# Kernel optimization log

Hardware: AMD Instinct MI355X
Metric: run time of the kernel (lower is better)

The kernel has to match this reference:

```python
import jax, jax.numpy as jnp
import numpy as np

NEMBED, EMBED_DIM, HID_DIM, OUT_DIM, NUM_CLASSES = 128, 64, 128, 128, 2
BATCH, TEAM = 2048, 5
N_OPS = 8


def setup_inputs() -> dict:
    key = jax.random.key(0)
    ks = jax.random.split(key, 8)
    w_eq = np.sqrt(2.0 / (EMBED_DIM + HID_DIM + N_OPS))
    return {
        "x": jax.random.randint(ks[0], (BATCH, 2, TEAM), 0, NEMBED, dtype=jnp.int32),
        "embed": jax.random.normal(ks[1], (NEMBED, EMBED_DIM), jnp.float32) * 0.1,
        "coefs1": jax.random.normal(ks[2], (EMBED_DIM, HID_DIM, N_OPS), jnp.float32) * w_eq,
        "bias1": jnp.zeros((HID_DIM,), jnp.float32),
        "wout1": jax.random.normal(ks[3], (HID_DIM, OUT_DIM), jnp.float32) * np.sqrt(1.0 / HID_DIM),
        "bout1": jnp.zeros((OUT_DIM,), jnp.float32),
        "coefs2": jax.random.normal(ks[4], (EMBED_DIM, HID_DIM, N_OPS), jnp.float32) * w_eq,
        "bias2": jnp.zeros((HID_DIM,), jnp.float32),
        "wout2": jax.random.normal(ks[5], (HID_DIM, OUT_DIM), jnp.float32) * np.sqrt(1.0 / HID_DIM),
        "bout2": jnp.zeros((OUT_DIM,), jnp.float32),
        "fcw": jax.random.normal(ks[6], (2 * OUT_DIM, NCLS := NUM_CLASSES and 2 * OUT_DIM and NUM_CLASSES), jnp.float32) * np.sqrt(1.0 / (2 * OUT_DIM)),
        "fcb": jnp.zeros((NUM_CLASSES,), jnp.float32),
    }


def eset_ops_3_to_3(t):
    # t: (N, D, m, m, m). 8 equivariant basis ops: keep-or-(sum&broadcast) each axis.
    # Pooled ops are kept with singleton dims; broadcasting happens after the
    # channel contraction (cheaper, same math as expand-then-contract).
    s1 = t.sum(-3, keepdims=True)
    s2 = t.sum(-2, keepdims=True)
    s3 = t.sum(-1, keepdims=True)
    s12 = t.sum((-3, -2), keepdims=True)
    s13 = t.sum((-3, -1), keepdims=True)
    s23 = t.sum((-2, -1), keepdims=True)
    sall = t.sum((-3, -2, -1), keepdims=True)
    return [t, s1, s2, s3, s12, s13, s23, sall]


def eq3_layer(t, coefs, bias):
    # coefs: (D_in, D_out, 8); output (N, D_out, m, m, m)
    ops = eset_ops_3_to_3(t)
    out = 0.0
    for b, op in enumerate(ops):
        out = out + jnp.einsum('ndijk,ds->nsijk', op, coefs[:, :, b])
    return out + bias[None, :, None, None, None]


def setnet3to3(t, coefs, bias, wout, bout):
    h = jax.nn.relu(eq3_layer(t, coefs, bias))          # (N, H, m, m, m)
    return jnp.einsum('nsijk,so->nijko', h, wout) + bout  # (N, m, m, m, out_dim)


def reference(x, embed, coefs1, bias1, wout1, bout1, coefs2, bias2, wout2, bout2, fcw, fcb):
    e1 = jax.nn.relu(embed[x[:, 0]])  # (N, 5, D)
    e2 = jax.nn.relu(embed[x[:, 1]])
    t1 = jnp.einsum('bid,bjd,bkd->bdijk', e1, e1, e1)  # (N, D, 5, 5, 5)
    t2 = jnp.einsum('bid,bjd,bkd->bdijk', e2, e2, e2)
    o1 = setnet3to3(t1, coefs1, bias1, wout1, bout1)
    o2 = setnet3to3(t2, coefs2, bias2, wout2, bout2)
    t1e = jax.nn.relu(o1.mean(axis=(1, 2, 3)))  # (N, out_dim)
    t2e = jax.nn.relu(o2.mean(axis=(1, 2, 3)))
    z = jnp.concatenate([t1e, t2e], axis=-1)    # dropout_prob=0 / eval mode: no-op
    return z @ fcw + fcb
```

## Files before the change

### kernel.cpp

```cpp
#include <hip/hip_runtime.h>


typedef __attribute__((ext_vector_type(8))) short bf16x8;
typedef __attribute__((ext_vector_type(4))) float f32x4;

#define DEV __device__ __forceinline__

DEV constexpr int pid2(int a, int b) {
  int x = a < b ? a : b;
  int y = a < b ? b : a;
  return x * (9 - x) / 2 + y;
}
DEV constexpr int tid3(int i, int j, int k) {
  int a = i, b = j, c = k, t;
  if (a > b) { t = a; a = b; b = t; }
  if (b > c) { t = b; b = c; c = t; }
  if (a > b) { t = a; a = b; b = t; }
  return a * (a * a - 18 * a + 107) / 6 + (b - a) * (11 - a - b) / 2 + (c - b);
}

DEV ushort f2bf(float f) {
  unsigned u = __builtin_bit_cast(unsigned, f);
  return (ushort)((u + 0x7FFFu + ((u >> 16) & 1u)) >> 16);
}

__global__ __launch_bounds__(256)
void cvt_coefs_kernel(const float* __restrict__ c1, const float* __restrict__ c2,
                      ushort* __restrict__ ct) {
  const int idx = blockIdx.x * 256 + threadIdx.x;
  const int d    = idx & 63;
  const int s    = (idx >> 6) & 127;
  const int b    = (idx >> 13) & 7;
  const int side = idx >> 16;
  const float* src = side ? c2 : c1;
  ct[idx] = f2bf(src[(d * 128 + s) * 8 + b]);
}


__global__ __launch_bounds__(256, 2)
void dota2_eq3_mfma(const int* __restrict__ x, const float* __restrict__ embed,
                    const float* __restrict__ bias1, const float* __restrict__ wout1,
                    const float* __restrict__ bout1,
                    const float* __restrict__ bias2, const float* __restrict__ wout2,
                    const float* __restrict__ bout2,
                    const float* __restrict__ fcw, const float* __restrict__ fcb,
                    const ushort* __restrict__ ct, float* __restrict__ out)
{
  __shared__ __align__(16) ushort FT[2][80][72];
  __shared__ __align__(16) float  OUT[128][100];
  __shared__ float hbarL[2][128];
  __shared__ float zL[256];

  const int n   = blockIdx.x;
  const int tid = threadIdx.x;
  const int w   = tid >> 6;
  const int l   = tid & 63;
  const int grp = l >> 4;
  const int lc  = l & 15;

  {
    unsigned long long* f8 = (unsigned long long*)&FT[0][0][0];
    #pragma unroll 4
    for (int i = tid; i < 2880; i += 256) f8[i] = 0ULL;
  }
  __syncthreads();

  if ((tid & 127) < 64) {
    const int side = tid >> 7;
    const int d = tid & 63;
    const int* xn = x + n * 10 + side * 5;
    float v[5];
    #pragma unroll
    for (int i = 0; i < 5; ++i) v[i] = fmaxf(embed[xn[i] * 64 + d], 0.f);
    const float S  = v[0] + v[1] + v[2] + v[3] + v[4];
    const float S2 = S * S;
    const float S3 = S2 * S;
    float p2[15];
    {
      int c2 = 0;
      #pragma unroll
      for (int a = 0; a < 5; ++a)
        #pragma unroll
        for (int b = a; b < 5; ++b) { p2[c2] = v[a] * v[b]; ++c2; }
    }
    ushort* colp = &FT[side][0][d];
    {
      int c3 = 0;
      #pragma unroll
      for (int a = 0; a < 5; ++a)
        #pragma unroll
        for (int b = a; b < 5; ++b)
          #pragma unroll
          for (int c = b; c < 5; ++c) { colp[c3 * 72] = f2bf(p2[pid2(a, b)] * v[c]); ++c3; }
    }
    #pragma unroll
    for (int t = 0; t < 15; ++t) colp[(48 + t) * 72] = f2bf(S * p2[t]);
    #pragma unroll
    for (int i = 0; i < 5; ++i)  colp[(64 + i) * 72] = f2bf(S2 * v[i]);
    colp[69 * 72] = f2bf(S3);
  }
  __syncthreads();

  #pragma unroll 1
  for (int side = 0; side < 2; ++side) {
    const ushort* CTs = ct + side * (8 * 128 * 64);

    auto afrag = [&](int b, int s0, int h) -> bf16x8 {
      const ushort* rp = CTs + (b * 128 + s0 + lc) * 64;
      return *(const bf16x8*)(rp + 32 * h + 8 * grp);
    };
    auto bfrag = [&](int t0, int h) -> bf16x8 {
      return *(const bf16x8*)(&FT[side][t0 + lc][32 * h + 8 * grp]);
    };
    auto dwrite = [&](const f32x4& acc, int s0, int colbase, int nvalid) {
      if (lc < nvalid) {
        float* p = &OUT[s0 + 4 * grp][colbase + lc];
        p[0] = acc[0]; p[100] = acc[1]; p[200] = acc[2]; p[300] = acc[3];
      }
    };

    {
      const bf16x8 A00 = afrag(0, 32 * w,      0), A01 = afrag(0, 32 * w,      1);
      const bf16x8 A10 = afrag(0, 32 * w + 16, 0), A11 = afrag(0, 32 * w + 16, 1);
      #pragma unroll
      for (int nt = 0; nt < 3; ++nt) {
        const bf16x8 B0 = bfrag(nt * 16, 0), B1 = bfrag(nt * 16, 1);
        const int nvalid = (nt == 2) ? 3 : 16;
        f32x4 acc0 = {0.f, 0.f, 0.f, 0.f};
        acc0 = __builtin_amdgcn_mfma_f32_16x16x32_bf16(A00, B0, acc0, 0, 0, 0);
        acc0 = __builtin_amdgcn_mfma_f32_16x16x32_bf16(A01, B1, acc0, 0, 0, 0);
        dwrite(acc0, 32 * w, nt * 16, nvalid);
        f32x4 acc1 = {0.f, 0.f, 0.f, 0.f};
        acc1 = __builtin_amdgcn_mfma_f32_16x16x32_bf16(A10, B0, acc1, 0, 0, 0);
        acc1 = __builtin_amdgcn_mfma_f32_16x16x32_bf16(A11, B1, acc1, 0, 0, 0);
        dwrite(acc1, 32 * w + 16, nt * 16, nvalid);
      }
    }
    {
      const bf16x8 B0 = bfrag(48, 0), B1 = bfrag(48, 1);
      #pragma unroll
      for (int b = 1; b <= 3; ++b)
        #pragma unroll
        for (int u = 0; u < 2; ++u) {
          const int s0 = 32 * w + 16 * u;
          const bf16x8 A0 = afrag(b, s0, 0), A1 = afrag(b, s0, 1);
          f32x4 acc = {0.f, 0.f, 0.f, 0.f};
          acc = __builtin_amdgcn_mfma_f32_16x16x32_bf16(A0, B0, acc, 0, 0, 0);
          acc = __builtin_amdgcn_mfma_f32_16x16x32_bf16(A1, B1, acc, 0, 0, 0);
          dwrite(acc, s0, 35 + (b - 1) * 15, 15);
        }
    }
    {
      const bf16x8 B0 = bfrag(64, 0), B1 = bfrag(64, 1);
      #pragma unroll
      for (int b = 4; b <= 6; ++b)
        #pragma unroll
        for (int u = 0; u < 2; ++u) {
          const int s0 = 32 * w + 16 * u;
          const bf16x8 A0 = afrag(b, s0, 0), A1 = afrag(b, s0, 1);
          f32x4 acc = {0.f, 0.f, 0.f, 0.f};
          acc = __builtin_amdgcn_mfma_f32_16x16x32_bf16(A0, B0, acc, 0, 0, 0);
          acc = __builtin_amdgcn_mfma_f32_16x16x32_bf16(A1, B1, acc, 0, 0, 0);
          dwrite(acc, s0, 80 + (b - 4) * 5, 5);
        }
      #pragma unroll
      for (int u = 0; u < 2; ++u) {
        const int s0 = 32 * w + 16 * u;
        const bf16x8 A0 = afrag(7, s0, 0), A1 = afrag(7, s0, 1);
        f32x4 acc = {0.f, 0.f, 0.f, 0.f};
        acc = __builtin_amdgcn_mfma_f32_16x16x32_bf16(A0, B0, acc, 0, 0, 0);
        acc = __builtin_amdgcn_mfma_f32_16x16x32_bf16(A1, B1, acc, 0, 0, 0);
        if (lc == 5) {
          float* p = &OUT[s0 + 4 * grp][95];
          p[0] = acc[0]; p[100] = acc[1]; p[200] = acc[2]; p[300] = acc[3];
        }
      }
    }
    __syncthreads();

    if (tid < 128) {
      const int s = tid;
      float T[96];
      const f32x4* rp = (const f32x4*)(&OUT[s][0]);
      #pragma unroll
      for (int j = 0; j < 24; ++j) {
        const f32x4 q = rp[j];
        T[4 * j] = q[0]; T[4 * j + 1] = q[1]; T[4 * j + 2] = q[2]; T[4 * j + 3] = q[3];
      }
      const float* bi = side ? bias2 : bias1;
      const float base = T[95] + bi[s];
      float hsum = 0.f;
      #pragma unroll
      for (int i = 0; i < 5; ++i) {
        const float pi = base + T[90 + i];
        #pragma unroll
        for (int j = 0; j < 5; ++j) {
          const float pij = pi + T[85 + j] + T[65 + pid2(i, j)];
          #pragma unroll
          for (int k = 0; k < 5; ++k) {
            const float val = pij + T[80 + k] + T[50 + pid2(i, k)] + T[35 + pid2(j, k)]
                            + T[tid3(i, j, k)];
            hsum += fmaxf(val, 0.f);
          }
        }
      }
      hbarL[side][s] = hsum * (1.f / 125.f);
    }
    __syncthreads();
  }

  {
    const int side = tid >> 7;
    const int o = tid & 127;
    const float* W  = side ? wout2 : wout1;
    const float* bo = side ? bout2 : bout1;
    const float* hb = &hbarL[side][0];
    float a0 = 0.f, a1 = 0.f, a2 = 0.f, a3 = 0.f;
    #pragma unroll 4
    for (int ss = 0; ss < 128; ss += 4) {
      a0 = fmaf(hb[ss + 0], W[(ss + 0) * 128 + o], a0);
      a1 = fmaf(hb[ss + 1], W[(ss + 1) * 128 + o], a1);
      a2 = fmaf(hb[ss + 2], W[(ss + 2) * 128 + o], a2);
      a3 = fmaf(hb[ss + 3], W[(ss + 3) * 128 + o], a3);
    }
    zL[side * 128 + o] = fmaxf(bo[o] + ((a0 + a1) + (a2 + a3)), 0.f);
  }
  __syncthreads();

  if (tid < 64) {
    const float4 zq = *reinterpret_cast<const float4*>(&zL[tid * 4]);
    const int q = tid * 4;
    float p0 = 0.f, p1 = 0.f;
    p0 = fmaf(zq.x, fcw[(q + 0) * 2 + 0], p0);
    p1 = fmaf(zq.x, fcw[(q + 0) * 2 + 1], p1);
    p0 = fmaf(zq.y, fcw[(q + 1) * 2 + 0], p0);
    p1 = fmaf(zq.y, fcw[(q + 1) * 2 + 1], p1);
    p0 = fmaf(zq.z, fcw[(q + 2) * 2 + 0], p0);
    p1 = fmaf(zq.z, fcw[(q + 2) * 2 + 1], p1);
    p0 = fmaf(zq.w, fcw[(q + 3) * 2 + 0], p0);
    p1 = fmaf(zq.w, fcw[(q + 3) * 2 + 1], p1);
    #pragma unroll
    for (int off = 32; off; off >>= 1) {
      p0 += __shfl_down(p0, off);
      p1 += __shfl_down(p1, off);
    }
    if (tid == 0) {
      out[n * 2 + 0] = p0 + fcb[0];
      out[n * 2 + 1] = p1 + fcb[1];
    }
  }
}

extern "C" void kernel_launch(void* const* d_in, const int* in_sizes, int n_in,
                              void* d_out, int out_size, void* d_ws, size_t ws_size,
                              hipStream_t stream) {
  const int*   x      = (const int*)  d_in[0];
  const float* embed  = (const float*)d_in[1];
  const float* coefs1 = (const float*)d_in[2];
  const float* bias1  = (const float*)d_in[3];
  const float* wout1  = (const float*)d_in[4];
  const float* bout1  = (const float*)d_in[5];
  const float* coefs2 = (const float*)d_in[6];
  const float* bias2  = (const float*)d_in[7];
  const float* wout2  = (const float*)d_in[8];
  const float* bout2  = (const float*)d_in[9];
  const float* fcw    = (const float*)d_in[10];
  const float* fcb    = (const float*)d_in[11];
  float* out  = (float*)d_out;
  ushort* ct  = (ushort*)d_ws;

  const int batch = in_sizes[0] / 10;
  cvt_coefs_kernel<<<512, 256, 0, stream>>>(coefs1, coefs2, ct);
  dota2_eq3_mfma<<<batch, 256, 0, stream>>>(
      x, embed, bias1, wout1, bout1, bias2, wout2, bout2, fcw, fcb, ct, out);
}
```

Measured before the change: 95.94 us.

## Split assembly across all threads, drop FT zeroing pass, pre-transpose wout

The 125-cell ReLU assembly is now split between two thread halves (62/63 cells each) that write partial sums to shared memory, so all 256 threads work instead of 128. The separate FT-wide zeroing loop and its barrier are removed; only the pad rows are zeroed inside the feature-building threads. The prep kernel also writes a transposed copy of wout into the workspace, so each output thread can read contiguous float4 vectors for the final matvec. In exchange there are extra barriers and a reduction step per side, plus a larger prep kernel launch.

```diff
diff --git a/kernel.cpp b/kernel.cpp
--- a/kernel.cpp
+++ b/kernel.cpp
@@ -25,15 +25,26 @@
 }
 
 __global__ __launch_bounds__(256)
-void cvt_coefs_kernel(const float* __restrict__ c1, const float* __restrict__ c2,
-                      ushort* __restrict__ ct) {
+void cvt_prep_kernel(const float* __restrict__ c1, const float* __restrict__ c2,
+                     const float* __restrict__ w1, const float* __restrict__ w2,
+                     ushort* __restrict__ ct, float* __restrict__ wt, int do_wt) {
   const int idx = blockIdx.x * 256 + threadIdx.x;
-  const int d    = idx & 63;
-  const int s    = (idx >> 6) & 127;
-  const int b    = (idx >> 13) & 7;
-  const int side = idx >> 16;
-  const float* src = side ? c2 : c1;
-  ct[idx] = f2bf(src[(d * 128 + s) * 8 + b]);
+  if (idx < 2 * 8 * 128 * 64) {
+    const int d    = idx & 63;
+    const int s    = (idx >> 6) & 127;
+    const int b    = (idx >> 13) & 7;
+    const int side = idx >> 16;
+    const float* src = side ? c2 : c1;
+    ct[idx] = f2bf(src[(d * 128 + s) * 8 + b]);
+  } else if (do_wt) {
+    const int j = idx - 131072;
+    if (j < 2 * 128 * 128) {
+      const int ss   = j & 127;
+      const int o    = (j >> 7) & 127;
+      const int side = j >> 14;
+      wt[j] = (side ? w2 : w1)[ss * 128 + o];
+    }
+  }
 }
 
 
@@ -44,12 +55,14 @@
                     const float* __restrict__ bias2, const float* __restrict__ wout2,
                     const float* __restrict__ bout2,
                     const float* __restrict__ fcw, const float* __restrict__ fcb,
-                    const ushort* __restrict__ ct, float* __restrict__ out)
+                    const ushort* __restrict__ ct, const float* __restrict__ wt,
+                    float* __restrict__ out)
 {
   __shared__ __align__(16) ushort FT[2][80][72];
   __shared__ __align__(16) float  OUT[128][100];
-  __shared__ float hbarL[2][128];
-  __shared__ float zL[256];
+  __shared__ __align__(16) float  PS[2][128];
+  __shared__ __align__(16) float  hbarL[2][128];
+  __shared__ __align__(16) float  zL[256];
 
   const int n   = blockIdx.x;
   const int tid = threadIdx.x;
@@ -58,15 +71,8 @@
   const int grp = l >> 4;
   const int lc  = l & 15;
 
-  {
-    unsigned long long* f8 = (unsigned long long*)&FT[0][0][0];
-    #pragma unroll 4
-    for (int i = tid; i < 2880; i += 256) f8[i] = 0ULL;
-  }
-  __syncthreads();
-
-  if ((tid & 127) < 64) {
-    const int side = tid >> 7;
+  if (tid < 128) {
+    const int side = tid >> 6;
     const int d = tid & 63;
     const int* xn = x + n * 10 + side * 5;
     float v[5];
@@ -98,33 +104,36 @@
     #pragma unroll
     for (int i = 0; i < 5; ++i)  colp[(64 + i) * 72] = f2bf(S2 * v[i]);
     colp[69 * 72] = f2bf(S3);
+    #pragma unroll
+    for (int r = 35; r < 48; ++r) colp[r * 72] = 0;
+    colp[63 * 72] = 0;
+    #pragma unroll
+    for (int r = 70; r < 80; ++r) colp[r * 72] = 0;
   }
   __syncthreads();
 
-  #pragma unroll 1
-  for (int side = 0; side < 2; ++side) {
+  auto bfrag = [&](int side, int t0, int h) -> bf16x8 {
+    return *(const bf16x8*)(&FT[side][t0 + lc][32 * h + 8 * grp]);
+  };
+  auto dwrite = [&](const f32x4& acc, int s0, int colbase, int nvalid) {
+    if (lc < nvalid) {
+      float* p = &OUT[s0 + 4 * grp][colbase + lc];
+      p[0] = acc[0]; p[100] = acc[1]; p[200] = acc[2]; p[300] = acc[3];
+    }
+  };
+
+  auto do_gemms = [&](int side) {
     const ushort* CTs = ct + side * (8 * 128 * 64);
-
     auto afrag = [&](int b, int s0, int h) -> bf16x8 {
       const ushort* rp = CTs + (b * 128 + s0 + lc) * 64;
       return *(const bf16x8*)(rp + 32 * h + 8 * grp);
     };
-    auto bfrag = [&](int t0, int h) -> bf16x8 {
-      return *(const bf16x8*)(&FT[side][t0 + lc][32 * h + 8 * grp]);
-    };
-    auto dwrite = [&](const f32x4& acc, int s0, int colbase, int nvalid) {
-      if (lc < nvalid) {
-        float* p = &OUT[s0 + 4 * grp][colbase + lc];
-        p[0] = acc[0]; p[100] = acc[1]; p[200] = acc[2]; p[300] = acc[3];
-      }
-    };
-
     {
       const bf16x8 A00 = afrag(0, 32 * w,      0), A01 = afrag(0, 32 * w,      1);
       const bf16x8 A10 = afrag(0, 32 * w + 16, 0), A11 = afrag(0, 32 * w + 16, 1);
       #pragma unroll
       for (int nt = 0; nt < 3; ++nt) {
-        const bf16x8 B0 = bfrag(nt * 16, 0), B1 = bfrag(nt * 16, 1);
+        const bf16x8 B0 = bfrag(side, nt * 16, 0), B1 = bfrag(side, nt * 16, 1);
         const int nvalid = (nt == 2) ? 3 : 16;
         f32x4 acc0 = {0.f, 0.f, 0.f, 0.f};
         acc0 = __builtin_amdgcn_mfma_f32_16x16x32_bf16(A00, B0, acc0, 0, 0, 0);
@@ -137,7 +146,7 @@
       }
     }
     {
-      const bf16x8 B0 = bfrag(48, 0), B1 = bfrag(48, 1);
+      const bf16x8 B0 = bfrag(side, 48, 0), B1 = bfrag(side, 48, 1);
       #pragma unroll
       for (int b = 1; b <= 3; ++b)
         #pragma unroll
@@ -151,7 +160,7 @@
         }
     }
     {
-      const bf16x8 B0 = bfrag(64, 0), B1 = bfrag(64, 1);
+      const bf16x8 B0 = bfrag(side, 64, 0), B1 = bfrag(side, 64, 1);
       #pragma unroll
       for (int b = 4; b <= 6; ++b)
         #pragma unroll
@@ -176,54 +185,83 @@
         }
       }
     }
-    __syncthreads();
-
-    if (tid < 128) {
-      const int s = tid;
-      float T[96];
-      const f32x4* rp = (const f32x4*)(&OUT[s][0]);
-      #pragma unroll
-      for (int j = 0; j < 24; ++j) {
-        const f32x4 q = rp[j];
-        T[4 * j] = q[0]; T[4 * j + 1] = q[1]; T[4 * j + 2] = q[2]; T[4 * j + 3] = q[3];
-      }
-      const float* bi = side ? bias2 : bias1;
-      const float base = T[95] + bi[s];
-      float hsum = 0.f;
-      #pragma unroll
-      for (int i = 0; i < 5; ++i) {
-        const float pi = base + T[90 + i];
-        #pragma unroll
-        for (int j = 0; j < 5; ++j) {
-          const float pij = pi + T[85 + j] + T[65 + pid2(i, j)];
-          #pragma unroll
-          for (int k = 0; k < 5; ++k) {
-            const float val = pij + T[80 + k] + T[50 + pid2(i, k)] + T[35 + pid2(j, k)]
-                            + T[tid3(i, j, k)];
-            hsum += fmaxf(val, 0.f);
-          }
-        }
-      }
-      hbarL[side][s] = hsum * (1.f / 125.f);
-    }
-    __syncthreads();
-  }
+  };
+
+  auto do_assembly = [&](int side) {
+    const int g2 = tid >> 7;
+    const int s  = tid & 127;
+    float T[96];
+    const f32x4* rp = (const f32x4*)(&OUT[s][0]);
+    #pragma unroll
+    for (int j = 0; j < 24; ++j) {
+      const f32x4 q = rp[j];
+      T[4 * j] = q[0]; T[4 * j + 1] = q[1]; T[4 * j + 2] = q[2]; T[4 * j + 3] = q[3];
+    }
+    const float* bi = side ? bias2 : bias1;
+    const float base = T[95] + bi[s];
+    float hsum = 0.f;
+    auto cell = [&](int c) {
+      const int i = c / 25, j = (c / 5) % 5, k = c % 5;
+      const float val = base + T[90 + i] + T[85 + j] + T[65 + pid2(i, j)]
+                      + T[80 + k] + T[50 + pid2(i, k)] + T[35 + pid2(j, k)]
+                      + T[tid3(i, j, k)];
+      hsum += fmaxf(val, 0.f);
+    };
+    if (g2 == 0) {
+      #pragma unroll
+      for (int c = 0; c < 62; ++c) cell(c);
+    } else {
+      #pragma unroll
+      for (int c = 62; c < 125; ++c) cell(c);
+    }
+    PS[g2][s] = hsum;
+  };
+
+  do_gemms(0);
+  __syncthreads();
+  do_assembly(0);
+  __syncthreads();
+  if (tid < 128) hbarL[0][tid] = (PS[0][tid] + PS[1][tid]) * (1.f / 125.f);
+  do_gemms(1);
+  __syncthreads();
+  do_assembly(1);
+  __syncthreads();
+  if (tid < 128) hbarL[1][tid] = (PS[0][tid] + PS[1][tid]) * (1.f / 125.f);
+  __syncthreads();
 
   {
     const int side = tid >> 7;
     const int o = tid & 127;
-    const float* W  = side ? wout2 : wout1;
     const float* bo = side ? bout2 : bout1;
-    const float* hb = &hbarL[side][0];
-    float a0 = 0.f, a1 = 0.f, a2 = 0.f, a3 = 0.f;
-    #pragma unroll 4
-    for (int ss = 0; ss < 128; ss += 4) {
-      a0 = fmaf(hb[ss + 0], W[(ss + 0) * 128 + o], a0);
-      a1 = fmaf(hb[ss + 1], W[(ss + 1) * 128 + o], a1);
-      a2 = fmaf(hb[ss + 2], W[(ss + 2) * 128 + o], a2);
-      a3 = fmaf(hb[ss + 3], W[(ss + 3) * 128 + o], a3);
-    }
-    zL[side * 128 + o] = fmaxf(bo[o] + ((a0 + a1) + (a2 + a3)), 0.f);
+    float r;
+    if (wt != nullptr) {
+      const f32x4* wv = (const f32x4*)(wt + (side << 14) + o * 128);
+      const f32x4* hv = (const f32x4*)(&hbarL[side][0]);
+      float a0 = 0.f, a1 = 0.f, a2 = 0.f, a3 = 0.f;
+      #pragma unroll 8
+      for (int q = 0; q < 32; ++q) {
+        const f32x4 wq = wv[q];
+        const f32x4 hq = hv[q];
+        a0 = fmaf(hq[0], wq[0], a0);
+        a1 = fmaf(hq[1], wq[1], a1);
+        a2 = fmaf(hq[2], wq[2], a2);
+        a3 = fmaf(hq[3], wq[3], a3);
+      }
+      r = (a0 + a1) + (a2 + a3);
+    } else {
+      const float* W = side ? wout2 : wout1;
+      const float* hb = &hbarL[side][0];
+      float a0 = 0.f, a1 = 0.f, a2 = 0.f, a3 = 0.f;
+      #pragma unroll 4
+      for (int ss = 0; ss < 128; ss += 4) {
+        a0 = fmaf(hb[ss + 0], W[(ss + 0) * 128 + o], a0);
+        a1 = fmaf(hb[ss + 1], W[(ss + 1) * 128 + o], a1);
+        a2 = fmaf(hb[ss + 2], W[(ss + 2) * 128 + o], a2);
+        a3 = fmaf(hb[ss + 3], W[(ss + 3) * 128 + o], a3);
+      }
+      r = (a0 + a1) + (a2 + a3);
+    }
+    zL[side * 128 + o] = fmaxf(bo[o] + r, 0.f);
   }
   __syncthreads();
 
@@ -267,10 +305,13 @@
   const float* fcw    = (const float*)d_in[10];
   const float* fcb    = (const float*)d_in[11];
   float* out  = (float*)d_out;
-  ushort* ct  = (ushort*)d_ws;
+
+  ushort* ct = (ushort*)d_ws;
+  const int do_wt = (ws_size >= (262144 + 131072)) ? 1 : 0;
+  float* wt = do_wt ? (float*)((char*)d_ws + 262144) : nullptr;
 
   const int batch = in_sizes[0] / 10;
-  cvt_coefs_kernel<<<512, 256, 0, stream>>>(coefs1, coefs2, ct);
+  cvt_prep_kernel<<<640, 256, 0, stream>>>(coefs1, coefs2, wout1, wout2, ct, wt, do_wt);
   dota2_eq3_mfma<<<batch, 256, 0, stream>>>(
-      x, embed, bias1, wout1, bout1, bias2, wout2, bout2, fcw, fcb, ct, out);
-}
+      x, embed, bias1, wout1, bout1, bias2, wout2, bout2, fcw, fcb, ct, wt, out);
+}
```

After: 108.9 us. +13.5%, slower.
